# Performance work log

Hardware: AMD Instinct MI355X
Metric: run time of the kernel (lower is better)

## Reference

```python
import jax, jax.numpy as jnp
import numpy as np

N_NODES = 1_000_000
N_EDGES = 4_000_000  # knn_k = 4
N_GRAPHS = 1024
HIDDEN = 64
N_FEAT = 4


def setup_inputs() -> dict:
    key = jax.random.key(0)
    k0, k1, k2, k3, k4 = jax.random.split(key, 5)
    x = jax.random.normal(k0, (N_NODES, N_FEAT), dtype=jnp.float32)
    edge_index = jax.random.randint(k1, (2, N_EDGES), 0, N_NODES, dtype=jnp.int64)
    batch = jnp.sort(jax.random.randint(k2, (N_NODES,), 0, N_GRAPHS, dtype=jnp.int64))
    W1 = jax.random.normal(k3, (N_FEAT, HIDDEN), dtype=jnp.float32) * 0.5
    b1 = jnp.zeros((HIDDEN,), dtype=jnp.float32)
    W2 = jax.random.normal(k4, (HIDDEN, 1), dtype=jnp.float32) * 0.1
    b2 = jnp.zeros((1,), dtype=jnp.float32)
    return {"x": x, "W1": W1, "b1": b1, "W2": W2, "b2": b2,
            "edge_index": edge_index, "batch": batch}


def gcn_conv(x, edge_index, W, b):
    # PyG GCNConv: linear transform, add self-loops, sym-normalize, scatter-add.
    n = x.shape[0]
    h = x @ W  # [N, 64]
    loop = jnp.arange(n, dtype=edge_index.dtype)
    row = jnp.concatenate([edge_index[0], loop])  # source j
    col = jnp.concatenate([edge_index[1], loop])  # target i
    deg = jax.ops.segment_sum(jnp.ones_like(col, dtype=h.dtype), col, num_segments=n)
    dis = jnp.where(deg > 0, jax.lax.rsqrt(jnp.maximum(deg, 1.0)), 0.0)
    norm = dis[row] * dis[col]  # [E+N]
    out = jax.ops.segment_sum(h[row] * norm[:, None], col, num_segments=n)
    return out + b


def reference(x, W1, b1, W2, b2, edge_index, batch):
    h = gcn_conv(x, edge_index, W1, b1)          # [N, 64]
    h = jax.nn.elu(h)                            # ELU activation
    pooled = jax.ops.segment_sum(h, batch, num_segments=N_GRAPHS)  # global_add_pool
    return pooled @ W2 + b2                      # [G, 1]
```

## Files before the change

kernel.cpp:

```cpp
#include <hip/hip_runtime.h>
#include <hip/hip_fp16.h>

#define N_NODES 1000000
#define N_EDGES 4000000
#define N_GRAPHS 1024
#define HIDDEN 64

#define G1 256
#define T1 512
#define EPB (N_EDGES / G1)
#define BSHIFT 11
#define BSIZE 2048
#define NBK 512
#define NBUCK ((N_NODES + BSIZE - 1) / BSIZE)

__global__ __launch_bounds__(T1) void k_hist(const int* __restrict__ col,
                                             int* __restrict__ part,
                                             float* __restrict__ out,
                                             const float* __restrict__ b2) {
    __shared__ int h[NBK];
    int t = threadIdx.x, blk = blockIdx.x;
    for (int i = t; i < NBK; i += T1) h[i] = 0;
    int gid = blk * T1 + t;
    if (gid < N_GRAPHS) out[gid] = b2[0];
    __syncthreads();
    int e0 = blk * EPB;
    for (int i = t; i < EPB; i += T1) {
        int c = col[e0 + i];
        atomicAdd(&h[c >> BSHIFT], 1);
    }
    __syncthreads();
    for (int i = t; i < NBK; i += T1) part[blk * NBK + i] = h[i];
}

__global__ __launch_bounds__(1024) void k_off(int* __restrict__ part,
                                              int* __restrict__ ebase,
                                              int* __restrict__ ecnt) {
    __shared__ int tot[2][NBK];
    __shared__ int sc[NBK];
    __shared__ int base[NBK];
    int t = threadIdx.x;
    int q = t >> 9;
    int b = t & (NBK - 1);
    int run = 0;
    for (int k = 0; k < G1 / 2; ++k) {
        int blk = q * (G1 / 2) + k;
        int v = part[blk * NBK + b];
        part[blk * NBK + b] = run;
        run += v;
    }
    tot[q][b] = run;
    __syncthreads();
    if (q == 0) {
        int t0 = tot[0][b], t1 = tot[1][b];
        ecnt[b] = t0 + t1;
        tot[0][b] = 0;
        tot[1][b] = t0;
        sc[b] = t0 + t1;
    }
    __syncthreads();
    for (int o = 1; o < NBK; o <<= 1) {
        int v = (q == 0 && b >= o) ? sc[b - o] : 0;
        __syncthreads();
        if (q == 0) sc[b] += v;
        __syncthreads();
    }
    if (q == 0) {
        base[b] = sc[b] - ecnt[b];
        ebase[b] = base[b];
    }
    __syncthreads();
    int add = tot[q][b] + base[b];
    for (int k = 0; k < G1 / 2; ++k) {
        int blk = q * (G1 / 2) + k;
        part[blk * NBK + b] += add;
    }
}

__global__ __launch_bounds__(T1) void k_part(const int* __restrict__ row,
                                             const int* __restrict__ col,
                                             const int* __restrict__ part,
                                             unsigned* __restrict__ epair) {
    __shared__ int cur[NBK];
    int t = threadIdx.x, blk = blockIdx.x;
    for (int i = t; i < NBK; i += T1) cur[i] = part[blk * NBK + i];
    __syncthreads();
    int e0 = blk * EPB;
    for (int i = t; i < EPB; i += T1) {
        int c = col[e0 + i];
        int r = row[e0 + i];
        int b = c >> BSHIFT;
        int pos = atomicAdd(&cur[b], 1);
        epair[pos] = ((unsigned)(c & (BSIZE - 1)) << 20) | (unsigned)r;
    }
}

__global__ __launch_bounds__(256) void k_deg2(const unsigned* __restrict__ epair,
                                              const int* __restrict__ ebase,
                                              const int* __restrict__ ecnt,
                                              const float4* __restrict__ x,
                                              float* __restrict__ dis,
                                              uint2* __restrict__ xdh) {
    __shared__ int deg[BSIZE];
    int t = threadIdx.x, b = blockIdx.x;
    for (int i = t; i < BSIZE; i += 256) deg[i] = 1;
    __syncthreads();
    int e0 = ebase[b], ne = ecnt[b];
    for (int i = t; i < ne; i += 256) {
        unsigned u = epair[e0 + i];
        atomicAdd(&deg[u >> 20], 1);
    }
    __syncthreads();
    int n0 = b << BSHIFT;
    for (int i = t; i < BSIZE; i += 256) {
        int node = n0 + i;
        if (node < N_NODES) {
            float d = rsqrtf((float)deg[i]);
            dis[node] = d;
            float4 xv = x[node];
            __half2 h01 = __floats2half2_rn(xv.x * d, xv.y * d);
            __half2 h23 = __floats2half2_rn(xv.z * d, xv.w * d);
            uint2 pk;
            pk.x = *(unsigned*)&h01;
            pk.y = *(unsigned*)&h23;
            xdh[node] = pk;
        }
    }
}

__device__ __forceinline__ void acc_edge(unsigned u, uint2 p, float* sf) {
    int loc = u >> 20;
    __half2 h01 = *(__half2*)&p.x;
    __half2 h23 = *(__half2*)&p.y;
    float2 f01 = __half22float2(h01);
    float2 f23 = __half22float2(h23);
    float* sp = sf + loc * 5;
    atomicAdd(sp + 0, f01.x);
    atomicAdd(sp + 1, f01.y);
    atomicAdd(sp + 2, f23.x);
    atomicAdd(sp + 3, f23.y);
}

__global__ __launch_bounds__(1024) void k_acc(const unsigned* __restrict__ epair,
                                              const int* __restrict__ ebase,
                                              const int* __restrict__ ecnt,
                                              const uint2* __restrict__ xdh,
                                              float4* __restrict__ sbuf) {
    __shared__ float sf[BSIZE * 5];
    int t = threadIdx.x, b = blockIdx.x;
    for (int i = t; i < BSIZE * 5; i += 1024) sf[i] = 0.f;
    __syncthreads();
    int e0 = ebase[b], ne = ecnt[b];
    int ne4 = ne & ~3;
    const unsigned* ep = epair + e0;
    for (int i = 4 * t; i < ne4; i += 4096) {
        unsigned u0 = ep[i], u1 = ep[i + 1], u2 = ep[i + 2], u3 = ep[i + 3];
        uint2 p0 = xdh[u0 & 0xFFFFFu];
        uint2 p1 = xdh[u1 & 0xFFFFFu];
        uint2 p2 = xdh[u2 & 0xFFFFFu];
        uint2 p3 = xdh[u3 & 0xFFFFFu];
        acc_edge(u0, p0, sf);
        acc_edge(u1, p1, sf);
        acc_edge(u2, p2, sf);
        acc_edge(u3, p3, sf);
    }
    for (int i = ne4 + t; i < ne; i += 1024) {
        unsigned u = ep[i];
        acc_edge(u, xdh[u & 0xFFFFFu], sf);
    }
    __syncthreads();
    int n0 = b << BSHIFT;
    for (int i = t; i < BSIZE; i += 1024) {
        int node = n0 + i;
        if (node < N_NODES) {
            const float* sp = sf + i * 5;
            sbuf[node] = make_float4(sp[0], sp[1], sp[2], sp[3]);
        }
    }
}

__global__ __launch_bounds__(256) void k_mlp(const float4* __restrict__ sbuf,
                                             const uint2* __restrict__ xdh,
                                             const float* __restrict__ dis,
                                             const int* __restrict__ batch,
                                             const float* __restrict__ W1,
                                             const float* __restrict__ b1,
                                             const float* __restrict__ W2,
                                             float* __restrict__ out) {
    int n = blockIdx.x * blockDim.x + threadIdx.x;
    bool valid = n < N_NODES;
    float acc = 0.f;
    int g = -1;
    if (valid) {
        float4 sv = sbuf[n];
        uint2 p = xdh[n];
        __half2 h01 = *(__half2*)&p.x;
        __half2 h23 = *(__half2*)&p.y;
        float2 f01 = __half22float2(h01);
        float2 f23 = __half22float2(h23);
        float d = dis[n];
        float u0 = d * (sv.x + f01.x);
        float u1 = d * (sv.y + f01.y);
        float u2 = d * (sv.z + f23.x);
        float u3 = d * (sv.w + f23.y);
        g = batch[n];
        #pragma unroll
        for (int k = 0; k < HIDDEN; ++k) {
            float t = fmaf(u0, W1[k],
                      fmaf(u1, W1[HIDDEN + k],
                      fmaf(u2, W1[2 * HIDDEN + k],
                      fmaf(u3, W1[3 * HIDDEN + k], b1[k]))));
            float h = t > 0.f ? t : (__expf(t) - 1.f);
            acc = fmaf(h, W2[k], acc);
        }
    }
    unsigned long long rem = __ballot(valid);
    while (rem) {
        int leader = __ffsll(rem) - 1;
        int gl = __shfl(g, leader);
        bool mine = valid && (g == gl);
        unsigned long long mask = __ballot(mine);
        float v = mine ? acc : 0.f;
        #pragma unroll
        for (int o = 32; o; o >>= 1) v += __shfl_xor(v, o);
        if ((int)(threadIdx.x & 63) == leader) unsafeAtomicAdd(&out[gl], v);
        rem &= ~mask;
    }
}

__global__ __launch_bounds__(256) void k_init(int* __restrict__ deg, float4* __restrict__ s,
                                              float* __restrict__ out, const float* __restrict__ b2) {
    int i = blockIdx.x * blockDim.x + threadIdx.x;
    if (i < N_NODES) { deg[i] = 1; s[i] = make_float4(0.f, 0.f, 0.f, 0.f); }
    if (i < N_GRAPHS) out[i] = b2[0];
}
__global__ __launch_bounds__(256) void k_deg(const int* __restrict__ col, int* __restrict__ deg) {
    int e = blockIdx.x * blockDim.x + threadIdx.x;
    if (e < N_EDGES) atomicAdd(&deg[col[e]], 1);
}
__global__ __launch_bounds__(256) void k_dis(const int* __restrict__ deg, float* __restrict__ dis) {
    int i = blockIdx.x * blockDim.x + threadIdx.x;
    if (i < N_NODES) dis[i] = rsqrtf((float)deg[i]);
}
__global__ __launch_bounds__(256) void k_scatter(const int* __restrict__ row, const int* __restrict__ col,
                                                 const float4* __restrict__ x, const float* __restrict__ dis,
                                                 float* __restrict__ s) {
    int e = blockIdx.x * blockDim.x + threadIdx.x;
    if (e >= N_EDGES) return;
    int j = row[e], i = col[e];
    float dj = dis[j];
    float4 xj = x[j];
    float* sp = s + 4ll * (long long)i;
    unsafeAtomicAdd(sp + 0, xj.x * dj);
    unsafeAtomicAdd(sp + 1, xj.y * dj);
    unsafeAtomicAdd(sp + 2, xj.z * dj);
    unsafeAtomicAdd(sp + 3, xj.w * dj);
}
__global__ __launch_bounds__(256) void k_node(const float4* __restrict__ x, const float4* __restrict__ s,
                                              const float* __restrict__ dis, const int* __restrict__ batch,
                                              const float* __restrict__ W1, const float* __restrict__ b1,
                                              const float* __restrict__ W2, float* __restrict__ out) {
    int n = blockIdx.x * blockDim.x + threadIdx.x;
    bool valid = n < N_NODES;
    float acc = 0.f; int g = -1;
    if (valid) {
        float4 xn = x[n], sn = s[n];
        float di = dis[n], inv = di * di;
        float u0 = di * sn.x + inv * xn.x, u1 = di * sn.y + inv * xn.y;
        float u2 = di * sn.z + inv * xn.z, u3 = di * sn.w + inv * xn.w;
        g = batch[n];
        #pragma unroll
        for (int k = 0; k < HIDDEN; ++k) {
            float t = fmaf(u0, W1[k], fmaf(u1, W1[HIDDEN + k],
                      fmaf(u2, W1[2 * HIDDEN + k], fmaf(u3, W1[3 * HIDDEN + k], b1[k]))));
            float h = t > 0.f ? t : expm1f(t);
            acc = fmaf(h, W2[k], acc);
        }
    }
    unsigned long long rem = __ballot(valid);
    while (rem) {
        int leader = __ffsll(rem) - 1;
        int gl = __shfl(g, leader);
        bool mine = valid && (g == gl);
        unsigned long long mask = __ballot(mine);
        float v = mine ? acc : 0.f;
        #pragma unroll
        for (int o = 32; o; o >>= 1) v += __shfl_xor(v, o);
        if ((int)(threadIdx.x & 63) == leader) unsafeAtomicAdd(&out[gl], v);
        rem &= ~mask;
    }
}

extern "C" void kernel_launch(void* const* d_in, const int* in_sizes, int n_in,
                              void* d_out, int out_size, void* d_ws, size_t ws_size,
                              hipStream_t stream) {
    const float* x   = (const float*)d_in[0];
    const float* W1  = (const float*)d_in[1];
    const float* b1  = (const float*)d_in[2];
    const float* W2  = (const float*)d_in[3];
    const float* b2  = (const float*)d_in[4];
    const int*   ei  = (const int*)d_in[5];
    const int*   bat = (const int*)d_in[6];
    float* out = (float*)d_out;

    const int* row = ei;
    const int* col = ei + N_EDGES;
    char* ws = (char*)d_ws;

    size_t o_ep   = 0;
    size_t o_sb   = o_ep + 16000000;
    size_t o_xdh  = o_sb + 16000000;
    size_t o_dis  = o_xdh + 8000000;
    size_t o_part = o_dis + 4000000;
    size_t o_eb   = o_part + (size_t)G1 * NBK * 4;
    size_t o_ec   = o_eb + NBK * 4;
    size_t need   = o_ec + NBK * 4;

    if (ws_size >= need) {
        unsigned* epair = (unsigned*)(ws + o_ep);
        float4*   sbuf  = (float4*)(ws + o_sb);
        uint2*    xdh   = (uint2*)(ws + o_xdh);
        float*    dis   = (float*)(ws + o_dis);
        int*      part  = (int*)(ws + o_part);
        int*      ebase = (int*)(ws + o_eb);
        int*      ecnt  = (int*)(ws + o_ec);

        k_hist<<<G1, T1, 0, stream>>>(col, part, out, b2);
        k_off<<<1, 1024, 0, stream>>>(part, ebase, ecnt);
        k_part<<<G1, T1, 0, stream>>>(row, col, part, epair);
        k_deg2<<<NBUCK, 256, 0, stream>>>(epair, ebase, ecnt, (const float4*)x, dis, xdh);
        k_acc<<<NBUCK, 1024, 0, stream>>>(epair, ebase, ecnt, xdh, sbuf);
        k_mlp<<<(N_NODES + 255) / 256, 256, 0, stream>>>(sbuf, xdh, dis, bat, W1, b1, W2, out);
    } else {
        int nb_n = (N_NODES + 255) / 256;
        int nb_e = (N_EDGES + 255) / 256;
        int*    deg = (int*)(ws);
        float*  dis = (float*)(ws + (size_t)N_NODES * 4);
        float*  s   = (float*)(ws + (size_t)N_NODES * 8);
        float4* s4  = (float4*)s;
        k_init<<<nb_n, 256, 0, stream>>>(deg, s4, out, b2);
        k_deg<<<nb_e, 256, 0, stream>>>(col, deg);
        k_dis<<<nb_n, 256, 0, stream>>>(deg, dis);
        k_scatter<<<nb_e, 256, 0, stream>>>(row, col, (const float4*)x, dis, s);
        k_node<<<nb_n, 256, 0, stream>>>((const float4*)x, s4, dis, bat, W1, b1, W2, out);
    }
}
```

Baseline: 198.9 us.

## Fuse accumulation with MLP pooling, shrink buckets, vectorize edge loads

Merges the per-bucket neighbor accumulation kernel with the node MLP and pooling kernel, so the 16 MB intermediate sum buffer is no longer written and read back. Bucket size drops to 1024 nodes (1024 buckets), which doubles the number of blocks and halves shared memory per block. Bucket starts are padded to multiples of 4 so edge pairs can be read as uint4. Histogram, partition and degree kernels now load int4 and uint4, and the offset scan is simplified to one thread per bucket. The exponential-heavy MLP now runs inside the scatter kernel, which could raise register pressure there and lower occupancy.

```diff
diff --git a/kernel.cpp b/kernel.cpp
--- a/kernel.cpp
+++ b/kernel.cpp
@@ -6,15 +6,16 @@
 #define N_GRAPHS 1024
 #define HIDDEN 64
 
-#define G1 256
+#define G1 250
 #define T1 512
 #define EPB (N_EDGES / G1)
-#define BSHIFT 11
-#define BSIZE 2048
-#define NBK 512
+#define EPB4 (EPB / 4)
+#define BSHIFT 10
+#define BSIZE 1024
+#define NBK 1024
 #define NBUCK ((N_NODES + BSIZE - 1) / BSIZE)
 
-__global__ __launch_bounds__(T1) void k_hist(const int* __restrict__ col,
+__global__ __launch_bounds__(T1) void k_hist(const int4* __restrict__ col4,
                                              int* __restrict__ part,
                                              float* __restrict__ out,
                                              const float* __restrict__ b2) {
@@ -24,10 +25,13 @@
     int gid = blk * T1 + t;
     if (gid < N_GRAPHS) out[gid] = b2[0];
     __syncthreads();
-    int e0 = blk * EPB;
-    for (int i = t; i < EPB; i += T1) {
-        int c = col[e0 + i];
-        atomicAdd(&h[c >> BSHIFT], 1);
+    int b0 = blk * EPB4;
+    for (int i = t; i < EPB4; i += T1) {
+        int4 c = col4[b0 + i];
+        atomicAdd(&h[((unsigned)c.x) >> BSHIFT], 1);
+        atomicAdd(&h[((unsigned)c.y) >> BSHIFT], 1);
+        atomicAdd(&h[((unsigned)c.z) >> BSHIFT], 1);
+        atomicAdd(&h[((unsigned)c.w) >> BSHIFT], 1);
     }
     __syncthreads();
     for (int i = t; i < NBK; i += T1) part[blk * NBK + i] = h[i];
@@ -36,66 +40,53 @@
 __global__ __launch_bounds__(1024) void k_off(int* __restrict__ part,
                                               int* __restrict__ ebase,
                                               int* __restrict__ ecnt) {
-    __shared__ int tot[2][NBK];
     __shared__ int sc[NBK];
-    __shared__ int base[NBK];
-    int t = threadIdx.x;
-    int q = t >> 9;
-    int b = t & (NBK - 1);
+    int b = threadIdx.x;
     int run = 0;
-    for (int k = 0; k < G1 / 2; ++k) {
-        int blk = q * (G1 / 2) + k;
-        int v = part[blk * NBK + b];
-        part[blk * NBK + b] = run;
+    for (int k = 0; k < G1; ++k) {
+        int v = part[k * NBK + b];
+        part[k * NBK + b] = run;
         run += v;
     }
-    tot[q][b] = run;
-    __syncthreads();
-    if (q == 0) {
-        int t0 = tot[0][b], t1 = tot[1][b];
-        ecnt[b] = t0 + t1;
-        tot[0][b] = 0;
-        tot[1][b] = t0;
-        sc[b] = t0 + t1;
-    }
+    ecnt[b] = run;
+    int run4 = (run + 3) & ~3;
+    sc[b] = run4;
     __syncthreads();
     for (int o = 1; o < NBK; o <<= 1) {
-        int v = (q == 0 && b >= o) ? sc[b - o] : 0;
+        int v = (b >= o) ? sc[b - o] : 0;
         __syncthreads();
-        if (q == 0) sc[b] += v;
+        sc[b] += v;
         __syncthreads();
     }
-    if (q == 0) {
-        base[b] = sc[b] - ecnt[b];
-        ebase[b] = base[b];
-    }
-    __syncthreads();
-    int add = tot[q][b] + base[b];
-    for (int k = 0; k < G1 / 2; ++k) {
-        int blk = q * (G1 / 2) + k;
-        part[blk * NBK + b] += add;
-    }
-}
-
-__global__ __launch_bounds__(T1) void k_part(const int* __restrict__ row,
-                                             const int* __restrict__ col,
+    int base = sc[b] - run4;
+    ebase[b] = base;
+    for (int k = 0; k < G1; ++k) part[k * NBK + b] += base;
+}
+
+__global__ __launch_bounds__(T1) void k_part(const int4* __restrict__ row4,
+                                             const int4* __restrict__ col4,
                                              const int* __restrict__ part,
                                              unsigned* __restrict__ epair) {
     __shared__ int cur[NBK];
     int t = threadIdx.x, blk = blockIdx.x;
     for (int i = t; i < NBK; i += T1) cur[i] = part[blk * NBK + i];
     __syncthreads();
-    int e0 = blk * EPB;
-    for (int i = t; i < EPB; i += T1) {
-        int c = col[e0 + i];
-        int r = row[e0 + i];
-        int b = c >> BSHIFT;
-        int pos = atomicAdd(&cur[b], 1);
-        epair[pos] = ((unsigned)(c & (BSIZE - 1)) << 20) | (unsigned)r;
-    }
-}
-
-__global__ __launch_bounds__(256) void k_deg2(const unsigned* __restrict__ epair,
+    int b0 = blk * EPB4;
+    for (int i = t; i < EPB4; i += T1) {
+        int4 c = col4[b0 + i];
+        int4 r = row4[b0 + i];
+        int cc[4] = {c.x, c.y, c.z, c.w};
+        int rr[4] = {r.x, r.y, r.z, r.w};
+        #pragma unroll
+        for (int k = 0; k < 4; ++k) {
+            int b = ((unsigned)cc[k]) >> BSHIFT;
+            int pos = atomicAdd(&cur[b], 1);
+            epair[pos] = ((unsigned)(cc[k] & (BSIZE - 1)) << 20) | (unsigned)rr[k];
+        }
+    }
+}
+
+__global__ __launch_bounds__(512) void k_deg2(const unsigned* __restrict__ epair,
                                               const int* __restrict__ ebase,
                                               const int* __restrict__ ecnt,
                                               const float4* __restrict__ x,
@@ -103,16 +94,22 @@
                                               uint2* __restrict__ xdh) {
     __shared__ int deg[BSIZE];
     int t = threadIdx.x, b = blockIdx.x;
-    for (int i = t; i < BSIZE; i += 256) deg[i] = 1;
-    __syncthreads();
-    int e0 = ebase[b], ne = ecnt[b];
-    for (int i = t; i < ne; i += 256) {
-        unsigned u = epair[e0 + i];
-        atomicAdd(&deg[u >> 20], 1);
-    }
+    for (int i = t; i < BSIZE; i += 512) deg[i] = 1;
+    __syncthreads();
+    int ne = ecnt[b];
+    const unsigned* ep = epair + ebase[b];
+    int ne4 = ne & ~3;
+    for (int i = 4 * t; i < ne4; i += 2048) {
+        uint4 u = *(const uint4*)(ep + i);
+        atomicAdd(&deg[u.x >> 20], 1);
+        atomicAdd(&deg[u.y >> 20], 1);
+        atomicAdd(&deg[u.z >> 20], 1);
+        atomicAdd(&deg[u.w >> 20], 1);
+    }
+    for (int i = ne4 + t; i < ne; i += 512) atomicAdd(&deg[ep[i] >> 20], 1);
     __syncthreads();
     int n0 = b << BSHIFT;
-    for (int i = t; i < BSIZE; i += 256) {
+    for (int i = t; i < BSIZE; i += 512) {
         int node = n0 + i;
         if (node < N_NODES) {
             float d = rsqrtf((float)deg[i]);
@@ -141,90 +138,91 @@
     atomicAdd(sp + 3, f23.y);
 }
 
-__global__ __launch_bounds__(1024) void k_acc(const unsigned* __restrict__ epair,
+__global__ __launch_bounds__(512) void k_accF(const unsigned* __restrict__ epair,
                                               const int* __restrict__ ebase,
                                               const int* __restrict__ ecnt,
                                               const uint2* __restrict__ xdh,
-                                              float4* __restrict__ sbuf) {
+                                              const float* __restrict__ dis,
+                                              const int* __restrict__ batch,
+                                              const float* __restrict__ W1,
+                                              const float* __restrict__ b1,
+                                              const float* __restrict__ W2,
+                                              float* __restrict__ out) {
     __shared__ float sf[BSIZE * 5];
     int t = threadIdx.x, b = blockIdx.x;
-    for (int i = t; i < BSIZE * 5; i += 1024) sf[i] = 0.f;
-    __syncthreads();
-    int e0 = ebase[b], ne = ecnt[b];
-    int ne4 = ne & ~3;
-    const unsigned* ep = epair + e0;
-    for (int i = 4 * t; i < ne4; i += 4096) {
-        unsigned u0 = ep[i], u1 = ep[i + 1], u2 = ep[i + 2], u3 = ep[i + 3];
-        uint2 p0 = xdh[u0 & 0xFFFFFu];
-        uint2 p1 = xdh[u1 & 0xFFFFFu];
-        uint2 p2 = xdh[u2 & 0xFFFFFu];
-        uint2 p3 = xdh[u3 & 0xFFFFFu];
-        acc_edge(u0, p0, sf);
-        acc_edge(u1, p1, sf);
-        acc_edge(u2, p2, sf);
-        acc_edge(u3, p3, sf);
-    }
-    for (int i = ne4 + t; i < ne; i += 1024) {
+    for (int i = t; i < BSIZE * 5; i += 512) sf[i] = 0.f;
+    __syncthreads();
+    int ne = ecnt[b];
+    const unsigned* ep = epair + ebase[b];
+    int ne8 = ne & ~7;
+    for (int i = 8 * t; i < ne8; i += 4096) {
+        uint4 q0 = *(const uint4*)(ep + i);
+        uint4 q1 = *(const uint4*)(ep + i + 4);
+        uint2 p0 = xdh[q0.x & 0xFFFFFu];
+        uint2 p1 = xdh[q0.y & 0xFFFFFu];
+        uint2 p2 = xdh[q0.z & 0xFFFFFu];
+        uint2 p3 = xdh[q0.w & 0xFFFFFu];
+        uint2 p4 = xdh[q1.x & 0xFFFFFu];
+        uint2 p5 = xdh[q1.y & 0xFFFFFu];
+        uint2 p6 = xdh[q1.z & 0xFFFFFu];
+        uint2 p7 = xdh[q1.w & 0xFFFFFu];
+        acc_edge(q0.x, p0, sf);
+        acc_edge(q0.y, p1, sf);
+        acc_edge(q0.z, p2, sf);
+        acc_edge(q0.w, p3, sf);
+        acc_edge(q1.x, p4, sf);
+        acc_edge(q1.y, p5, sf);
+        acc_edge(q1.z, p6, sf);
+        acc_edge(q1.w, p7, sf);
+    }
+    for (int i = ne8 + t; i < ne; i += 512) {
         unsigned u = ep[i];
         acc_edge(u, xdh[u & 0xFFFFFu], sf);
     }
     __syncthreads();
     int n0 = b << BSHIFT;
-    for (int i = t; i < BSIZE; i += 1024) {
-        int node = n0 + i;
-        if (node < N_NODES) {
-            const float* sp = sf + i * 5;
-            sbuf[node] = make_float4(sp[0], sp[1], sp[2], sp[3]);
-        }
-    }
-}
-
-__global__ __launch_bounds__(256) void k_mlp(const float4* __restrict__ sbuf,
-                                             const uint2* __restrict__ xdh,
-                                             const float* __restrict__ dis,
-                                             const int* __restrict__ batch,
-                                             const float* __restrict__ W1,
-                                             const float* __restrict__ b1,
-                                             const float* __restrict__ W2,
-                                             float* __restrict__ out) {
-    int n = blockIdx.x * blockDim.x + threadIdx.x;
-    bool valid = n < N_NODES;
-    float acc = 0.f;
-    int g = -1;
-    if (valid) {
-        float4 sv = sbuf[n];
-        uint2 p = xdh[n];
-        __half2 h01 = *(__half2*)&p.x;
-        __half2 h23 = *(__half2*)&p.y;
-        float2 f01 = __half22float2(h01);
-        float2 f23 = __half22float2(h23);
-        float d = dis[n];
-        float u0 = d * (sv.x + f01.x);
-        float u1 = d * (sv.y + f01.y);
-        float u2 = d * (sv.z + f23.x);
-        float u3 = d * (sv.w + f23.y);
-        g = batch[n];
-        #pragma unroll
-        for (int k = 0; k < HIDDEN; ++k) {
-            float t = fmaf(u0, W1[k],
-                      fmaf(u1, W1[HIDDEN + k],
-                      fmaf(u2, W1[2 * HIDDEN + k],
-                      fmaf(u3, W1[3 * HIDDEN + k], b1[k]))));
-            float h = t > 0.f ? t : (__expf(t) - 1.f);
-            acc = fmaf(h, W2[k], acc);
-        }
-    }
-    unsigned long long rem = __ballot(valid);
-    while (rem) {
-        int leader = __ffsll(rem) - 1;
-        int gl = __shfl(g, leader);
-        bool mine = valid && (g == gl);
-        unsigned long long mask = __ballot(mine);
-        float v = mine ? acc : 0.f;
-        #pragma unroll
-        for (int o = 32; o; o >>= 1) v += __shfl_xor(v, o);
-        if ((int)(threadIdx.x & 63) == leader) unsafeAtomicAdd(&out[gl], v);
-        rem &= ~mask;
+    #pragma unroll
+    for (int k = 0; k < BSIZE / 512; ++k) {
+        int ln = t + k * 512;
+        int node = n0 + ln;
+        bool valid = node < N_NODES;
+        float acc = 0.f;
+        int g = -1;
+        if (valid) {
+            const float* sp = sf + ln * 5;
+            uint2 p = xdh[node];
+            __half2 h01 = *(__half2*)&p.x;
+            __half2 h23 = *(__half2*)&p.y;
+            float2 f01 = __half22float2(h01);
+            float2 f23 = __half22float2(h23);
+            float d = dis[node];
+            float u0 = d * (sp[0] + f01.x);
+            float u1 = d * (sp[1] + f01.y);
+            float u2 = d * (sp[2] + f23.x);
+            float u3 = d * (sp[3] + f23.y);
+            g = batch[node];
+            #pragma unroll
+            for (int kk = 0; kk < HIDDEN; ++kk) {
+                float tt = fmaf(u0, W1[kk],
+                           fmaf(u1, W1[HIDDEN + kk],
+                           fmaf(u2, W1[2 * HIDDEN + kk],
+                           fmaf(u3, W1[3 * HIDDEN + kk], b1[kk]))));
+                float h = tt > 0.f ? tt : (__expf(tt) - 1.f);
+                acc = fmaf(h, W2[kk], acc);
+            }
+        }
+        unsigned long long rem = __ballot(valid);
+        while (rem) {
+            int leader = __ffsll(rem) - 1;
+            int gl = __shfl(g, leader);
+            bool mine = valid && (g == gl);
+            unsigned long long mask = __ballot(mine);
+            float v = mine ? acc : 0.f;
+            #pragma unroll
+            for (int o = 32; o; o >>= 1) v += __shfl_xor(v, o);
+            if ((int)(t & 63) == leader) unsafeAtomicAdd(&out[gl], v);
+            rem &= ~mask;
+        }
     }
 }
 
@@ -308,29 +306,26 @@
     char* ws = (char*)d_ws;
 
     size_t o_ep   = 0;
-    size_t o_sb   = o_ep + 16000000;
-    size_t o_xdh  = o_sb + 16000000;
-    size_t o_dis  = o_xdh + 8000000;
-    size_t o_part = o_dis + 4000000;
+    size_t o_xdh  = o_ep + (size_t)(N_EDGES + 4 * NBK) * 4;
+    size_t o_dis  = o_xdh + (size_t)N_NODES * 8;
+    size_t o_part = o_dis + (size_t)N_NODES * 4;
     size_t o_eb   = o_part + (size_t)G1 * NBK * 4;
     size_t o_ec   = o_eb + NBK * 4;
     size_t need   = o_ec + NBK * 4;
 
     if (ws_size >= need) {
         unsigned* epair = (unsigned*)(ws + o_ep);
-        float4*   sbuf  = (float4*)(ws + o_sb);
         uint2*    xdh   = (uint2*)(ws + o_xdh);
         float*    dis   = (float*)(ws + o_dis);
         int*      part  = (int*)(ws + o_part);
         int*      ebase = (int*)(ws + o_eb);
         int*      ecnt  = (int*)(ws + o_ec);
 
-        k_hist<<<G1, T1, 0, stream>>>(col, part, out, b2);
+        k_hist<<<G1, T1, 0, stream>>>((const int4*)col, part, out, b2);
         k_off<<<1, 1024, 0, stream>>>(part, ebase, ecnt);
-        k_part<<<G1, T1, 0, stream>>>(row, col, part, epair);
-        k_deg2<<<NBUCK, 256, 0, stream>>>(epair, ebase, ecnt, (const float4*)x, dis, xdh);
-        k_acc<<<NBUCK, 1024, 0, stream>>>(epair, ebase, ecnt, xdh, sbuf);
-        k_mlp<<<(N_NODES + 255) / 256, 256, 0, stream>>>(sbuf, xdh, dis, bat, W1, b1, W2, out);
+        k_part<<<G1, T1, 0, stream>>>((const int4*)row, (const int4*)col, part, epair);
+        k_deg2<<<NBUCK, 512, 0, stream>>>(epair, ebase, ecnt, (const float4*)x, dis, xdh);
+        k_accF<<<NBUCK, 512, 0, stream>>>(epair, ebase, ecnt, xdh, dis, bat, W1, b1, W2, out);
     } else {
         int nb_n = (N_NODES + 255) / 256;
         int nb_e = (N_EDGES + 255) / 256;
```

Result: no change. 202.1 us (+1.6%).
